# Kernel optimization log

Measured on AMD Instinct MI355X. Metric: run time of the kernel, lower is better.

## Reference

```python
import jax, jax.numpy as jnp
import numpy as np

OMEGA = 0.1
DT = 0.1
ODE_UNFOLDS = 6
BATCH, UNITS, INPUT_DIM = 2048, 128, 128


def setup_inputs() -> dict:
    key = jax.random.key(0)
    k0, k1, k2, k3, k4 = jax.random.split(key, 5)
    lim = float(np.sqrt(6.0 / (UNITS + INPUT_DIM)))  # glorot_uniform bound
    inputs = jax.random.normal(k0, (BATCH, INPUT_DIM), jnp.float32)
    state = jax.random.normal(k1, (BATCH, UNITS), jnp.float32)
    A = jax.random.uniform(k2, (UNITS, INPUT_DIM), jnp.float32, -lim, lim)
    sigma = jax.random.uniform(k3, (UNITS, INPUT_DIM), jnp.float32, -lim, lim)
    mu = jax.random.uniform(k4, (UNITS, INPUT_DIM), jnp.float32, -lim, lim)
    return {"inputs": inputs, "state": state, "A": A, "sigma": sigma, "mu": mu}


def reference(inputs, state, A, sigma, mu):
    # ODECell.call with Euler unfolding.
    # f = sigmoid(sigma * (x_t - mu)) depends only on the (constant) inputs,
    # so it is identical every unfold step; compute it (and its reductions) once.
    # sum(f * (A - x[..., None]), -1) == sum(f*A, -1) - x * sum(f, -1)  (same math)
    dt_u = DT / ODE_UNFOLDS
    f = jax.nn.sigmoid(sigma[None, :, :] * (inputs[:, None, :] - mu[None, :, :]))  # (B,U,D)
    fA = jnp.sum(f * A[None, :, :], axis=-1)  # (B,U)
    fs = jnp.sum(f, axis=-1)                  # (B,U)
    x = state
    for _ in range(ODE_UNFOLDS):
        dx = -OMEGA * x + fA - x * fs
        x = x + dt_u * dx
    return x
```

## Files before the change

### kernel.cpp

```cpp
#include <hip/hip_runtime.h>
#include <hip/hip_bf16.h>


#define BATCH 2048
#define UNITS 128
#define IDIM  128
#define L2E   1.4426950408889634f

__global__ __launch_bounds__(256) void ode_prep(
    const float* __restrict__ inputs,
    const float* __restrict__ sigma,
    const float* __restrict__ mu,
    float* __restrict__ xT,
    float* __restrict__ P,
    float* __restrict__ Q)
{
    const int bx  = blockIdx.x;
    const int tid = threadIdx.x;
    if (bx < 256) {
        __shared__ float t[32][33];
        const int tileC = bx & 3;
        const int tileR = bx >> 2;
        const int c0 = tileC * 32, r0 = tileR * 32;
        const int tx = tid & 31, ty = tid >> 5;
        #pragma unroll
        for (int i = 0; i < 32; i += 8)
            t[ty + i][tx] = inputs[(r0 + ty + i) * IDIM + (c0 + tx)];
        __syncthreads();
        #pragma unroll
        for (int i = 0; i < 32; i += 8)
            xT[(c0 + ty + i) * BATCH + (r0 + tx)] = t[tx][ty + i];
    } else {
        const int i = (bx - 256) * 256 + tid;
        const float s = sigma[i];
        P[i] = -L2E * s;
        Q[i] =  L2E * s * mu[i];
    }
}

__global__ __launch_bounds__(256) void ode_main(
    const float* __restrict__ xT,
    const float* __restrict__ state,
    const float* __restrict__ A,
    const float* __restrict__ P,
    const float* __restrict__ Q,
    float* __restrict__ out)
{
    const int tid  = threadIdx.x;
    const int lane = tid & 63;
    const int wave = tid >> 6;
    const int bx   = blockIdx.x;
    const int b    = (bx & 31) * 64 + lane;
    int u          = (bx >> 5) * 4 + wave;
    u = __builtin_amdgcn_readfirstlane(u);

    const float* __restrict__ Pu = P + u * IDIM;
    const float* __restrict__ Qu = Q + u * IDIM;
    const float* __restrict__ Au = A + u * IDIM;

    float fA0 = 0.f, fA1 = 0.f, fs0 = 0.f, fs1 = 0.f;
    #pragma unroll 8
    for (int d = 0; d < IDIM; d += 2) {
        const float x0 = xT[d * BATCH + b];
        const float x1 = xT[(d + 1) * BATCH + b];
        const float p0 = Pu[d],     q0 = Qu[d],     a0 = Au[d];
        const float p1 = Pu[d + 1], q1 = Qu[d + 1], a1 = Au[d + 1];
        const float e0 = __builtin_amdgcn_exp2f(fmaf(p0, x0, q0));
        const float e1 = __builtin_amdgcn_exp2f(fmaf(p1, x1, q1));
        const float f0 = __builtin_amdgcn_rcpf(1.0f + e0);
        const float f1 = __builtin_amdgcn_rcpf(1.0f + e1);
        fA0 = fmaf(f0, a0, fA0);
        fA1 = fmaf(f1, a1, fA1);
        fs0 += f0;
        fs1 += f1;
    }
    const float fA = fA0 + fA1;
    const float fs = fs0 + fs1;

    float x = state[b * UNITS + u];
    const float dtu = (float)(0.1 / 6.0);
    const float ofs = 0.1f + fs;
    #pragma unroll
    for (int k = 0; k < 6; ++k) {
        const float dx = fmaf(-x, ofs, fA);
        x = fmaf(dtu, dx, x);
    }
    out[b * UNITS + u] = x;
}

extern "C" void kernel_launch(void* const* d_in, const int* in_sizes, int n_in,
                              void* d_out, int out_size, void* d_ws, size_t ws_size,
                              hipStream_t stream) {
    const float* inputs = (const float*)d_in[0];
    const float* state  = (const float*)d_in[1];
    const float* A      = (const float*)d_in[2];
    const float* sigma  = (const float*)d_in[3];
    const float* mu     = (const float*)d_in[4];
    float* out = (float*)d_out;

    float* xT = (float*)d_ws;
    float* P  = xT + BATCH * IDIM;
    float* Q  = P + UNITS * IDIM;

    ode_prep<<<320, 256, 0, stream>>>(inputs, sigma, mu, xT, P, Q);
    ode_main<<<1024, 256, 0, stream>>>(xT, state, A, P, Q, out);
}
```

Baseline: 74.87 us.

## Fuse prep into main kernel with LDS-staged inputs and two units per wave

Merges the transpose/precompute kernel into the main kernel. Each block stages a 64x128 input tile into padded LDS and precomputes the sigma/mu exponent coefficients for 8 units in LDS. Each wave then computes two units per lane, so every x value read is reused twice. This removes one launch and the global xT/P/Q round trip. In exchange each of 512 blocks reloads its input tile and recomputes the coefficients, and there are half as many blocks as before.

```diff
diff --git a/kernel.cpp b/kernel.cpp
--- a/kernel.cpp
+++ b/kernel.cpp
@@ -7,85 +7,102 @@
 #define IDIM  128
 #define L2E   1.4426950408889634f
 
-__global__ __launch_bounds__(256) void ode_prep(
+#define BTILE 64
+#define UTILE 8
+#define XPAD  132
+
+__global__ __launch_bounds__(256) void ode_fused(
     const float* __restrict__ inputs,
+    const float* __restrict__ state,
+    const float* __restrict__ A,
     const float* __restrict__ sigma,
     const float* __restrict__ mu,
-    float* __restrict__ xT,
-    float* __restrict__ P,
-    float* __restrict__ Q)
-{
-    const int bx  = blockIdx.x;
-    const int tid = threadIdx.x;
-    if (bx < 256) {
-        __shared__ float t[32][33];
-        const int tileC = bx & 3;
-        const int tileR = bx >> 2;
-        const int c0 = tileC * 32, r0 = tileR * 32;
-        const int tx = tid & 31, ty = tid >> 5;
-        #pragma unroll
-        for (int i = 0; i < 32; i += 8)
-            t[ty + i][tx] = inputs[(r0 + ty + i) * IDIM + (c0 + tx)];
-        __syncthreads();
-        #pragma unroll
-        for (int i = 0; i < 32; i += 8)
-            xT[(c0 + ty + i) * BATCH + (r0 + tx)] = t[tx][ty + i];
-    } else {
-        const int i = (bx - 256) * 256 + tid;
-        const float s = sigma[i];
-        P[i] = -L2E * s;
-        Q[i] =  L2E * s * mu[i];
-    }
-}
-
-__global__ __launch_bounds__(256) void ode_main(
-    const float* __restrict__ xT,
-    const float* __restrict__ state,
-    const float* __restrict__ A,
-    const float* __restrict__ P,
-    const float* __restrict__ Q,
     float* __restrict__ out)
 {
+    __shared__ float  xl[BTILE * XPAD];
+    __shared__ float2 pq[UTILE][IDIM];
+
     const int tid  = threadIdx.x;
     const int lane = tid & 63;
-    const int wave = tid >> 6;
+    const int wave = __builtin_amdgcn_readfirstlane(tid >> 6);
     const int bx   = blockIdx.x;
-    const int b    = (bx & 31) * 64 + lane;
-    int u          = (bx >> 5) * 4 + wave;
-    u = __builtin_amdgcn_readfirstlane(u);
+    const int b0   = (bx & 31) * BTILE;
+    const int u0   = (bx >> 5) * UTILE;
 
-    const float* __restrict__ Pu = P + u * IDIM;
-    const float* __restrict__ Qu = Q + u * IDIM;
-    const float* __restrict__ Au = A + u * IDIM;
+    {
+        const float4* in4 = (const float4*)(inputs + b0 * IDIM);
+        const int c4 = tid & 31;
+        int r = tid >> 5;
+        #pragma unroll
+        for (int k = 0; k < 8; ++k, r += 8) {
+            float4 v = in4[r * (IDIM / 4) + c4];
+            *(float4*)(xl + r * XPAD + c4 * 4) = v;
+        }
+    }
+    {
+        #pragma unroll
+        for (int k = 0; k < 4; ++k) {
+            const int idx = k * 256 + tid;
+            const int uu = idx >> 7, dd = idx & 127;
+            const float s = sigma[(u0 + uu) * IDIM + dd];
+            const float m = mu[(u0 + uu) * IDIM + dd];
+            pq[uu][dd] = make_float2(-L2E * s, L2E * s * m);
+        }
+    }
+    __syncthreads();
 
-    float fA0 = 0.f, fA1 = 0.f, fs0 = 0.f, fs1 = 0.f;
-    #pragma unroll 8
-    for (int d = 0; d < IDIM; d += 2) {
-        const float x0 = xT[d * BATCH + b];
-        const float x1 = xT[(d + 1) * BATCH + b];
-        const float p0 = Pu[d],     q0 = Qu[d],     a0 = Au[d];
-        const float p1 = Pu[d + 1], q1 = Qu[d + 1], a1 = Au[d + 1];
-        const float e0 = __builtin_amdgcn_exp2f(fmaf(p0, x0, q0));
-        const float e1 = __builtin_amdgcn_exp2f(fmaf(p1, x1, q1));
-        const float f0 = __builtin_amdgcn_rcpf(1.0f + e0);
-        const float f1 = __builtin_amdgcn_rcpf(1.0f + e1);
-        fA0 = fmaf(f0, a0, fA0);
-        fA1 = fmaf(f1, a1, fA1);
-        fs0 += f0;
-        fs1 += f1;
+    const int la = wave * 2, lb = la + 1;
+    const int ua = u0 + la, ub = u0 + lb;
+    const float* __restrict__ Aa = A + ua * IDIM;
+    const float* __restrict__ Ab = A + ub * IDIM;
+
+    float fAa0 = 0.f, fAa1 = 0.f, fsa0 = 0.f, fsa1 = 0.f;
+    float fAb0 = 0.f, fAb1 = 0.f, fsb0 = 0.f, fsb1 = 0.f;
+
+    const float* xrow = xl + lane * XPAD;
+    #pragma unroll 2
+    for (int d = 0; d < IDIM; d += 4) {
+        const float4 x4 = *(const float4*)(xrow + d);
+        const float4 pa01 = *(const float4*)&pq[la][d];
+        const float4 pa23 = *(const float4*)&pq[la][d + 2];
+        const float4 pb01 = *(const float4*)&pq[lb][d];
+        const float4 pb23 = *(const float4*)&pq[lb][d + 2];
+        const float4 a4a  = *(const float4*)(Aa + d);
+        const float4 a4b  = *(const float4*)(Ab + d);
+
+        const float fa0 = __builtin_amdgcn_rcpf(1.0f + __builtin_amdgcn_exp2f(fmaf(pa01.x, x4.x, pa01.y)));
+        const float fa1 = __builtin_amdgcn_rcpf(1.0f + __builtin_amdgcn_exp2f(fmaf(pa01.z, x4.y, pa01.w)));
+        const float fa2 = __builtin_amdgcn_rcpf(1.0f + __builtin_amdgcn_exp2f(fmaf(pa23.x, x4.z, pa23.y)));
+        const float fa3 = __builtin_amdgcn_rcpf(1.0f + __builtin_amdgcn_exp2f(fmaf(pa23.z, x4.w, pa23.w)));
+        const float fb0 = __builtin_amdgcn_rcpf(1.0f + __builtin_amdgcn_exp2f(fmaf(pb01.x, x4.x, pb01.y)));
+        const float fb1 = __builtin_amdgcn_rcpf(1.0f + __builtin_amdgcn_exp2f(fmaf(pb01.z, x4.y, pb01.w)));
+        const float fb2 = __builtin_amdgcn_rcpf(1.0f + __builtin_amdgcn_exp2f(fmaf(pb23.x, x4.z, pb23.y)));
+        const float fb3 = __builtin_amdgcn_rcpf(1.0f + __builtin_amdgcn_exp2f(fmaf(pb23.z, x4.w, pb23.w)));
+
+        fAa0 = fmaf(fa0, a4a.x, fAa0);  fAa1 = fmaf(fa1, a4a.y, fAa1);
+        fAa0 = fmaf(fa2, a4a.z, fAa0);  fAa1 = fmaf(fa3, a4a.w, fAa1);
+        fsa0 += fa0 + fa2;              fsa1 += fa1 + fa3;
+        fAb0 = fmaf(fb0, a4b.x, fAb0);  fAb1 = fmaf(fb1, a4b.y, fAb1);
+        fAb0 = fmaf(fb2, a4b.z, fAb0);  fAb1 = fmaf(fb3, a4b.w, fAb1);
+        fsb0 += fb0 + fb2;              fsb1 += fb1 + fb3;
     }
-    const float fA = fA0 + fA1;
-    const float fs = fs0 + fs1;
 
-    float x = state[b * UNITS + u];
+    const float fA_a = fAa0 + fAa1, fs_a = fsa0 + fsa1;
+    const float fA_b = fAb0 + fAb1, fs_b = fsb0 + fsb1;
+
+    const int b = b0 + lane;
+    float xa = state[b * UNITS + ua];
+    float xb = state[b * UNITS + ub];
     const float dtu = (float)(0.1 / 6.0);
-    const float ofs = 0.1f + fs;
+    const float ofa = 0.1f + fs_a;
+    const float ofb = 0.1f + fs_b;
     #pragma unroll
     for (int k = 0; k < 6; ++k) {
-        const float dx = fmaf(-x, ofs, fA);
-        x = fmaf(dtu, dx, x);
+        xa = fmaf(dtu, fmaf(-xa, ofa, fA_a), xa);
+        xb = fmaf(dtu, fmaf(-xb, ofb, fA_b), xb);
     }
-    out[b * UNITS + u] = x;
+    out[b * UNITS + ua] = xa;
+    out[b * UNITS + ub] = xb;
 }
 
 extern "C" void kernel_launch(void* const* d_in, const int* in_sizes, int n_in,
@@ -98,10 +115,6 @@
     const float* mu     = (const float*)d_in[4];
     float* out = (float*)d_out;
 
-    float* xT = (float*)d_ws;
-    float* P  = xT + BATCH * IDIM;
-    float* Q  = P + UNITS * IDIM;
-
-    ode_prep<<<320, 256, 0, stream>>>(inputs, sigma, mu, xT, P, Q);
-    ode_main<<<1024, 256, 0, stream>>>(xT, state, A, P, Q, out);
+    ode_fused<<<(BATCH / BTILE) * (UNITS / UTILE), 256, 0, stream>>>(
+        inputs, state, A, sigma, mu, out);
 }
```

Measured after the change: 70.51 us. 5.8% less time.
